# Performance work log

Hardware: AMD Instinct MI355X
Metric: run time of the kernel (lower is better)

Reference implementation:

```python
import jax, jax.numpy as jnp
import numpy as np

U, I, N, E, F, H, TOPK = 2048, 16384, 18432, 1_000_000, 64, 32, 3
NEG = -1e30  # stands in for 'structural zero' entries excluded from top-k


def setup_inputs() -> dict:
    key = jax.random.key(0)
    ks = jax.random.split(key, 6)
    x = jax.random.normal(ks[0], (N, F), dtype=jnp.float32)
    w1 = jax.random.normal(ks[1], (H, 2 * F + 2), dtype=jnp.float32) * 0.1
    b1 = jnp.zeros((H,), dtype=jnp.float32)
    w2 = jax.random.normal(ks[2], (1, H), dtype=jnp.float32) * 0.1
    b2 = jnp.zeros((1,), dtype=jnp.float32)
    edge_src = jax.random.randint(ks[3], (E,), 0, U)        # user-local == global (user_idx = arange)
    edge_dst_item = jax.random.randint(ks[4], (E,), 0, I)   # item-local; global item id = U + item
    user_idx = jnp.arange(U, dtype=jnp.int64) if jax.config.jax_enable_x64 else jnp.arange(U, dtype=jnp.int32)
    return {"x": x, "w1": w1, "b1": b1, "w2": w2, "b2": b2,
            "edge_src": edge_src, "edge_dst_item": edge_dst_item,
            "user_idx": user_idx, "num_nodes": N}


def reference(x, w1, b1, w2, b2, edge_src, edge_dst_item, user_idx, num_nodes):
    num_users = user_idx.shape[0]
    num_items = num_nodes - num_users
    u_local = edge_src           # user_idx = arange(U) so user_map is identity
    i_local = edge_dst_item      # item nodes occupy indices [U, N)

    ones = jnp.ones(u_local.shape[0], dtype=jnp.float32)
    d_u = jnp.log1p(jax.ops.segment_sum(ones, u_local, num_segments=num_users))  # [U]
    d_i = jnp.log1p(jax.ops.segment_sum(ones, i_local, num_segments=num_items))  # [I]

    # per-edge features: [u_x, log1p(deg_u), i_x, log1p(deg_i)] -> [E, 2F+2]
    x_u = x[user_idx[u_local]]
    x_it = x[num_users + i_local]
    x_e = jnp.concatenate([x_u, d_u[u_local][:, None], x_it, d_i[i_local][:, None]], axis=1)
    h = jax.nn.relu(x_e @ w1.T + b1)
    w = jax.nn.sigmoid(h @ w2.T + b2)[:, 0]  # [E], edge weights in (0,1)

    # A' [U, I] (duplicate edges coalesce-summed), C = A' A'^T with degree scaling
    A = jnp.zeros((num_users, num_items), dtype=jnp.float32).at[u_local, i_local].add(w)
    C = A @ A.T
    Dh = jnp.sqrt(d_u)
    C = C * Dh[:, None] * Dh[None, :]

    # per-row top-k restricted to structural nonzeros (all weights > 0)
    Cm = jnp.where(C > 0, C, NEG)
    vals, idx = jax.lax.top_k(Cm, TOPK)          # [U, K]
    valid = vals > 0
    vhalf = jnp.where(valid, vals, 0.0) * 0.5
    rows = jnp.broadcast_to(jnp.arange(num_users)[:, None], (num_users, TOPK))
    T = jnp.zeros((num_users, num_users), dtype=jnp.float32).at[rows, idx].add(vhalf)
    S = T + T.T  # symmetrized, deduped-by-sum adjacency; S[r,c] = val of edge (r,c)
    return S, d_u
```

## Files before the change

kernel.cpp:

```cpp
#include <hip/hip_runtime.h>
#include <hip/hip_bf16.h>
#include <math.h>

#define U_N 2048
#define I_N 16384
#define F_N 64
#define H_N 32
#define KDIM 16384
#define NEGV (-1e30f)
#define NB_DEG 256

typedef __attribute__((ext_vector_type(4))) float f32x4;

__device__ __forceinline__ void gload16(const void* g, void* l) {
    __builtin_amdgcn_global_load_lds(
        (const __attribute__((address_space(1))) unsigned int*)g,
        (__attribute__((address_space(3))) unsigned int*)l, 16, 0, 0);
}

__global__ __launch_bounds__(256) void k_deg_part(const int* __restrict__ src,
                                                  const int* __restrict__ dst, int E,
                                                  unsigned int* __restrict__ pu,
                                                  unsigned int* __restrict__ pi2,
                                                  float* __restrict__ C,
                                                  float* __restrict__ out) {
    __shared__ unsigned int hu[U_N];
    __shared__ unsigned int hi2[I_N / 2];
    int tid = threadIdx.x;
    for (int t = tid; t < U_N; t += 256) hu[t] = 0u;
    for (int t = tid; t < I_N / 2; t += 256) hi2[t] = 0u;
    __syncthreads();
    const int4* s4 = (const int4*)src;
    const int4* d4 = (const int4*)dst;
    int nv = E >> 2;
    for (int v = blockIdx.x * 256 + tid; v < nv; v += NB_DEG * 256) {
        int4 u = s4[v], i = d4[v];
        atomicAdd(&hu[u.x], 1u); atomicAdd(&hi2[i.x >> 1], 1u << ((i.x & 1) * 16));
        atomicAdd(&hu[u.y], 1u); atomicAdd(&hi2[i.y >> 1], 1u << ((i.y & 1) * 16));
        atomicAdd(&hu[u.z], 1u); atomicAdd(&hi2[i.z >> 1], 1u << ((i.z & 1) * 16));
        atomicAdd(&hu[u.w], 1u); atomicAdd(&hi2[i.w >> 1], 1u << ((i.w & 1) * 16));
    }
    if (blockIdx.x == 0) {
        int e = nv * 4 + tid;
        if (e < E) {
            atomicAdd(&hu[src[e]], 1u);
            int i = dst[e];
            atomicAdd(&hi2[i >> 1], 1u << ((i & 1) * 16));
        }
    }
    __syncthreads();
    unsigned int* pub = pu + (size_t)blockIdx.x * U_N;
    unsigned int* pib = pi2 + (size_t)blockIdx.x * (I_N / 2);
    for (int t = tid; t < U_N; t += 256) pub[t] = hu[t];
    for (int t = tid; t < I_N / 2; t += 256) pib[t] = hi2[t];
    const float4 z4 = {0.f, 0.f, 0.f, 0.f};
    float4* C4 = (float4*)C;
    for (int t = blockIdx.x * 256 + tid; t < U_N * U_N / 4; t += NB_DEG * 256)
        C4[t] = z4;
    float4* o4 = (float4*)out;
    for (int t = blockIdx.x * 256 + tid; t < (U_N * U_N + U_N) / 4; t += NB_DEG * 256)
        o4[t] = z4;
}

__global__ __launch_bounds__(256) void k_node2(const unsigned int* __restrict__ pu,
                                               const unsigned int* __restrict__ pi2,
                                               float* __restrict__ du,
                                               float* __restrict__ di,
                                               float* __restrict__ Dh,
                                               float* __restrict__ out_du,
                                               unsigned int* __restrict__ degu) {
    __shared__ unsigned int red[8][32];
    int j = threadIdx.x >> 5, l = threadIdx.x & 31;
    int e = blockIdx.x * 32 + l;
    unsigned int s = 0;
    if (e < U_N) {
        const unsigned int* p = pu + e;
#pragma unroll
        for (int k = 0; k < 32; ++k) s += p[(size_t)(j * 32 + k) * U_N];
    } else {
        const unsigned int* p = pi2 + (e - U_N);
#pragma unroll
        for (int k = 0; k < 32; ++k) s += p[(size_t)(j * 32 + k) * (I_N / 2)];
    }
    red[j][l] = s;
    __syncthreads();
    if (threadIdx.x < 32) {
        unsigned int t = 0;
#pragma unroll
        for (int jj = 0; jj < 8; ++jj) t += red[jj][l];
        if (e < U_N) {
            degu[e] = t;
            float v = log1pf((float)t);
            du[e] = v;
            Dh[e] = sqrtf(v);
            out_du[e] = v;
        } else {
            int ii = e - U_N;
            di[2 * ii]     = log1pf((float)(t & 0xffffu));
            di[2 * ii + 1] = log1pf((float)(t >> 16));
        }
    }
}

__global__ __launch_bounds__(256) void k_pof(const unsigned int* __restrict__ pu,
                                             const unsigned int* __restrict__ degu,
                                             unsigned int* __restrict__ base,
                                             unsigned int* __restrict__ pof) {
    __shared__ unsigned int dg[U_N];
    __shared__ unsigned int wt[4];
    __shared__ unsigned int ps[8][32];
    int tid = threadIdx.x;
    int wave = tid >> 6, lane = tid & 63;
    for (int t = tid; t < U_N; t += 256) dg[t] = degu[t];
    __syncthreads();
    unsigned int loc[8];
    unsigned int s = 0;
#pragma unroll
    for (int j = 0; j < 8; ++j) { loc[j] = dg[tid * 8 + j]; s += loc[j]; }
    unsigned int inc = s;
#pragma unroll
    for (int off = 1; off < 64; off <<= 1) {
        unsigned int o = __shfl_up(inc, off);
        if (lane >= off) inc += o;
    }
    if (lane == 63) wt[wave] = inc;
    __syncthreads();
    unsigned int woff = 0;
#pragma unroll
    for (int w = 0; w < 4; ++w) woff += (w < wave) ? wt[w] : 0u;
    unsigned int ex = woff + inc - s;
    __syncthreads();
    {
        unsigned int run = ex;
#pragma unroll
        for (int j = 0; j < 8; ++j) { unsigned int v = loc[j]; dg[tid * 8 + j] = run; run += v; }
    }
    __syncthreads();
    int c = tid >> 5, l = tid & 31;
    int u = blockIdx.x * 32 + l;
    if (c == 0) base[u] = dg[u];
    unsigned int v32[32];
    unsigned int sum = 0;
#pragma unroll
    for (int k = 0; k < 32; ++k) {
        v32[k] = pu[(size_t)(c * 32 + k) * U_N + u];
        sum += v32[k];
    }
    ps[c][l] = sum;
    __syncthreads();
    unsigned int run = dg[u];
#pragma unroll
    for (int c2 = 0; c2 < 8; ++c2) run += (c2 < c) ? ps[c2][l] : 0u;
#pragma unroll
    for (int k = 0; k < 32; ++k) {
        pof[(size_t)(c * 32 + k) * U_N + u] = run;
        run += v32[k];
    }
}

#define NPROJ (((U_N + I_N) * H_N) / 256)
__global__ __launch_bounds__(256) void k_pe(const int* __restrict__ src,
                                            const int* __restrict__ dst, int E,
                                            const unsigned int* __restrict__ pof,
                                            unsigned short* __restrict__ sorted,
                                            const float* __restrict__ x,
                                            const float* __restrict__ w1,
                                            const float* __restrict__ b1,
                                            const float* __restrict__ du,
                                            const float* __restrict__ di,
                                            float* __restrict__ Pu,
                                            float* __restrict__ Pi) {
    __shared__ unsigned int cur[U_N];
    int tid = threadIdx.x;
    int bid = blockIdx.x;
    if (bid < NB_DEG) {
        const unsigned int* p = pof + (size_t)bid * U_N;
        for (int t = tid; t < U_N; t += 256) cur[t] = p[t];
        __syncthreads();
        const int4* s4 = (const int4*)src;
        const int4* d4 = (const int4*)dst;
        int nv = E >> 2;
        for (int v = bid * 256 + tid; v < nv; v += NB_DEG * 256) {
            int4 u = s4[v], i = d4[v];
            sorted[atomicAdd(&cur[u.x], 1u)] = (unsigned short)i.x;
            sorted[atomicAdd(&cur[u.y], 1u)] = (unsigned short)i.y;
            sorted[atomicAdd(&cur[u.z], 1u)] = (unsigned short)i.z;
            sorted[atomicAdd(&cur[u.w], 1u)] = (unsigned short)i.w;
        }
        if (bid == 0) {
            int e = nv * 4 + tid;
            if (e < E)
                sorted[atomicAdd(&cur[src[e]], 1u)] = (unsigned short)dst[e];
        }
    } else {
        int t = (bid - NB_DEG) * 256 + tid;
        if (t < U_N * H_N) {
            int u = t >> 5, j = t & 31;
            const float* xr = x + (size_t)u * F_N;
            const float* wr = w1 + (size_t)j * (2 * F_N + 2);
            float acc = b1[j] + du[u] * wr[64];
#pragma unroll
            for (int f = 0; f < F_N; ++f) acc = fmaf(xr[f], wr[f], acc);
            Pu[t] = acc;
        } else {
            int t2 = t - U_N * H_N;
            int i = t2 >> 5, j = t2 & 31;
            const float* xr = x + (size_t)(U_N + i) * F_N;
            const float* wr = w1 + (size_t)j * (2 * F_N + 2) + 65;
            float acc = di[i] * wr[64];
#pragma unroll
            for (int f = 0; f < F_N; ++f) acc = fmaf(xr[f], wr[f], acc);
            Pi[t2] = acc;
        }
    }
}

__global__ __launch_bounds__(256) void k_edge2(const unsigned short* __restrict__ sorted,
                                               const unsigned int* __restrict__ base,
                                               const unsigned int* __restrict__ degu,
                                               const float* __restrict__ Pu,
                                               const float* __restrict__ Pi,
                                               const float* __restrict__ w2,
                                               const float* __restrict__ b2,
                                               unsigned int* __restrict__ A8w,
                                               float* __restrict__ diag) {
    __shared__ float hrow[I_N];
    __shared__ float red[256];
    int u = blockIdx.x, tid = threadIdx.x;
    float4* h4 = (float4*)hrow;
    float4 z4 = {0.f, 0.f, 0.f, 0.f};
#pragma unroll
    for (int j = 0; j < 16; ++j) h4[tid + j * 256] = z4;

    float pur[H_N], w2r[H_N];
#pragma unroll
    for (int j = 0; j < H_N; ++j) pur[j] = Pu[(size_t)u * H_N + j];
#pragma unroll
    for (int j = 0; j < H_N; ++j) w2r[j] = w2[j];
    float bb = b2[0];
    __syncthreads();

    int nb = (int)base[u], d = (int)degu[u];
    for (int k = tid; k < d; k += 256) {
        int i = (int)sorted[nb + k];
        const float4* pi4 = (const float4*)(Pi + (size_t)i * H_N);
        float acc = bb;
#pragma unroll
        for (int q = 0; q < H_N / 4; ++q) {
            float4 b = pi4[q];
            acc = fmaf(fmaxf(pur[4 * q + 0] + b.x, 0.f), w2r[4 * q + 0], acc);
            acc = fmaf(fmaxf(pur[4 * q + 1] + b.y, 0.f), w2r[4 * q + 1], acc);
            acc = fmaf(fmaxf(pur[4 * q + 2] + b.z, 0.f), w2r[4 * q + 2], acc);
            acc = fmaf(fmaxf(pur[4 * q + 3] + b.w, 0.f), w2r[4 * q + 3], acc);
        }
        float wgt = 1.0f / (1.0f + expf(-acc));
        atomicAdd(&hrow[i], wgt);
    }
    __syncthreads();

    unsigned int* row = A8w + (size_t)u * (I_N / 4);
    float ss = 0.f;
#pragma unroll
    for (int j = 0; j < 16; ++j) {
        int w = tid + j * 256;
        float4 a = h4[w];
        int v = __builtin_amdgcn_cvt_pk_fp8_f32(a.x, a.y, 0, false);
        v = __builtin_amdgcn_cvt_pk_fp8_f32(a.z, a.w, v, true);
        row[w] = (unsigned int)v;
        ss = fmaf(a.x, a.x, ss); ss = fmaf(a.y, a.y, ss);
        ss = fmaf(a.z, a.z, ss); ss = fmaf(a.w, a.w, ss);
    }
    red[tid] = ss;
    __syncthreads();
#pragma unroll
    for (int s = 128; s > 0; s >>= 1) {
        if (tid < s) red[tid] += red[tid + s];
        __syncthreads();
    }
    if (tid == 0) diag[u] = red[0];
}

#define BM 128
#define BKB 128
#define NBLK (U_N / BM)
#define NPAIR (NBLK * (NBLK + 1) / 2)
#define KSPLIT 4
#define KCH (KDIM / KSPLIT)

__global__ __launch_bounds__(256) void k_syrk(const unsigned char* __restrict__ A8,
                                              float* __restrict__ C) {
    __shared__ unsigned char As[BM * BKB];
    __shared__ unsigned char Bs[BM * BKB];

    int k0 = blockIdx.x * KCH;
    int p = blockIdx.y;
    int bi = 0, rem = p;
    while (rem >= NBLK - bi) { rem -= NBLK - bi; ++bi; }
    int bj = bi + rem;
    int diagp = (bi == bj);

    int tid = threadIdx.x;
    int wave = tid >> 6, lane = tid & 63;

    int srow = wave * 32 + (lane >> 3);
    int scol = ((lane & 7) ^ (lane >> 3)) * 16;
    const unsigned char* Ag = A8 + (size_t)(bi * BM + srow) * KDIM + k0 + scol;
    const unsigned char* Bg = A8 + (size_t)(bj * BM + srow) * KDIM + k0 + scol;
    unsigned char* lA = As + (wave * 32) * BKB;
    unsigned char* lB = Bs + (wave * 32) * BKB;

    int wm = wave >> 1, wn = wave & 1;
    int lm = lane & 15, lq = lane >> 4;
    int lm7 = lm & 7;
    const unsigned char* bTile = diagp ? As : Bs;

    f32x4 acc[4][4];
#pragma unroll
    for (int m = 0; m < 4; ++m)
#pragma unroll
        for (int n = 0; n < 4; ++n) acc[m][n] = (f32x4){0.f, 0.f, 0.f, 0.f};

    for (int kt = 0; kt < KCH; kt += BKB) {
        __syncthreads();
#pragma unroll
        for (int j = 0; j < 4; ++j)
            gload16(Ag + kt + (size_t)(j * 8) * KDIM, lA + j * 8 * BKB);
        if (!diagp) {
#pragma unroll
            for (int j = 0; j < 4; ++j)
                gload16(Bg + kt + (size_t)(j * 8) * KDIM, lB + j * 8 * BKB);
        }
        __syncthreads();

#pragma unroll
        for (int s = 0; s < 4; ++s) {
            int off = ((s * 2 + (lq >> 1)) ^ lm7) * 16 + (lq & 1) * 8;
            long av[4], bv[4];
#pragma unroll
            for (int m = 0; m < 4; ++m)
                av[m] = *(const long*)(As + (wm * 64 + m * 16 + lm) * BKB + off);
#pragma unroll
            for (int n = 0; n < 4; ++n)
                bv[n] = *(const long*)(bTile + (wn * 64 + n * 16 + lm) * BKB + off);
#pragma unroll
            for (int m = 0; m < 4; ++m)
#pragma unroll
                for (int n = 0; n < 4; ++n)
                    acc[m][n] = __builtin_amdgcn_mfma_f32_16x16x32_fp8_fp8(
                        av[m], bv[n], acc[m][n], 0, 0, 0);
        }
    }

#pragma unroll
    for (int m = 0; m < 4; ++m) {
        int rb = bi * BM + wm * 64 + m * 16 + lq * 4;
#pragma unroll
        for (int n = 0; n < 4; ++n) {
            int c = bj * BM + wn * 64 + n * 16 + lm;
            f32x4 v = acc[m][n];
#pragma unroll
            for (int g = 0; g < 4; ++g)
                atomicAdd(&C[(size_t)(rb + g) * U_N + c], v[g]);
        }
    }
}

__global__ __launch_bounds__(256) void k_mirror(float* __restrict__ C) {
    __shared__ float T[64][65];
    int tr = blockIdx.x, tc = blockIdx.y;
    if ((tr >> 1) <= (tc >> 1)) return;
    int lane = threadIdx.x & 63;
    int w = threadIdx.x >> 6;
#pragma unroll
    for (int s = 0; s < 16; ++s) {
        int r = s * 4 + w;
        T[r][lane] = C[(size_t)(tc * 64 + r) * U_N + tr * 64 + lane];
    }
    __syncthreads();
#pragma unroll
    for (int s = 0; s < 16; ++s) {
        int r = s * 4 + w;
        C[(size_t)(tr * 64 + r) * U_N + tc * 64 + lane] = T[lane][r];
    }
}

__device__ __forceinline__ bool better(float va, int ia, float vb, int ib) {
    return (va > vb) || (va == vb && ia < ib);
}
__device__ __forceinline__ void ins3(float v, int i, float& v0, int& i0,
                                     float& v1, int& i1, float& v2, int& i2) {
    if (better(v, i, v0, i0)) { v2 = v1; i2 = i1; v1 = v0; i1 = i0; v0 = v; i0 = i; }
    else if (better(v, i, v1, i1)) { v2 = v1; i2 = i1; v1 = v; i1 = i; }
    else if (better(v, i, v2, i2)) { v2 = v; i2 = i; }
}

__global__ __launch_bounds__(256) void k_topk(const float* __restrict__ C,
                                              const float* __restrict__ Dh,
                                              const float* __restrict__ diag,
                                              float* __restrict__ out) {
    int wave = threadIdx.x >> 6, lane = threadIdx.x & 63;
    int r = blockIdx.x * 4 + wave;
    float dr = Dh[r];
    float dex = diag[r] * dr * dr;
    float dval = (dex > 0.f) ? dex : NEGV;
    const float4* row = (const float4*)(C + (size_t)r * U_N);
    const float4* dh4 = (const float4*)Dh;
    float v0 = NEGV, v1 = NEGV, v2 = NEGV;
    int i0 = 0x7fffffff, i1 = 0x7fffffff, i2 = 0x7fffffff;
    int qr = r >> 2;
    for (int q = lane; q < U_N / 4; q += 64) {
        float4 cv = row[q];
        float4 dv = dh4[q];
        int c = q * 4;
        float x0 = (cv.x > 0.f) ? cv.x * dr * dv.x : NEGV;
        float x1 = (cv.y > 0.f) ? cv.y * dr * dv.y : NEGV;
        float x2 = (cv.z > 0.f) ? cv.z * dr * dv.z : NEGV;
        float x3 = (cv.w > 0.f) ? cv.w * dr * dv.w : NEGV;
        if (q == qr) {
            int j = r & 3;
            if (j == 0) x0 = dval; else if (j == 1) x1 = dval;
            else if (j == 2) x2 = dval; else x3 = dval;
        }
        if (better(x0, c + 0, v2, i2)) ins3(x0, c + 0, v0, i0, v1, i1, v2, i2);
        if (better(x1, c + 1, v2, i2)) ins3(x1, c + 1, v0, i0, v1, i1, v2, i2);
        if (better(x2, c + 2, v2, i2)) ins3(x2, c + 2, v0, i0, v1, i1, v2, i2);
        if (better(x3, c + 3, v2, i2)) ins3(x3, c + 3, v0, i0, v1, i1, v2, i2);
    }
#pragma unroll
    for (int off = 1; off < 64; off <<= 1) {
        float ov0 = __shfl_xor(v0, off), ov1 = __shfl_xor(v1, off), ov2 = __shfl_xor(v2, off);
        int oi0 = __shfl_xor(i0, off), oi1 = __shfl_xor(i1, off), oi2 = __shfl_xor(i2, off);
        ins3(ov0, oi0, v0, i0, v1, i1, v2, i2);
        ins3(ov1, oi1, v0, i0, v1, i1, v2, i2);
        ins3(ov2, oi2, v0, i0, v1, i1, v2, i2);
    }
    if (lane == 0) {
        float vs[3] = {v0, v1, v2};
        int is[3] = {i0, i1, i2};
#pragma unroll
        for (int k = 0; k < 3; ++k) {
            if (vs[k] > 0.f) {
                atomicAdd(&out[(size_t)r * U_N + is[k]], 0.5f * vs[k]);
                atomicAdd(&out[(size_t)is[k] * U_N + r], 0.5f * vs[k]);
            }
        }
    }
}

extern "C" void kernel_launch(void* const* d_in, const int* in_sizes, int n_in,
                              void* d_out, int out_size, void* d_ws, size_t ws_size,
                              hipStream_t stream) {
    const float* x  = (const float*)d_in[0];
    const float* w1 = (const float*)d_in[1];
    const float* b1 = (const float*)d_in[2];
    const float* w2 = (const float*)d_in[3];
    const float* b2 = (const float*)d_in[4];
    const int* esrc = (const int*)d_in[5];
    const int* edst = (const int*)d_in[6];
    int E = in_sizes[5];
    float* out = (float*)d_out;

    unsigned char* A8 = (unsigned char*)d_ws;
    float* C    = (float*)(A8 + (size_t)U_N * I_N);
    float* Pu   = C + (size_t)U_N * U_N;
    float* Pi   = Pu + (size_t)U_N * H_N;
    unsigned int* pu  = (unsigned int*)(Pi + (size_t)I_N * H_N);
    unsigned int* pi2 = pu + (size_t)NB_DEG * U_N;
    unsigned int* pof = pi2 + (size_t)NB_DEG * (I_N / 2);
    unsigned int* degu = pof + (size_t)NB_DEG * U_N;
    unsigned int* base = degu + U_N;
    float* du   = (float*)(base + U_N);
    float* di   = du + U_N;
    float* Dh   = di + I_N;
    float* diag = Dh + U_N;
    unsigned short* sorted = (unsigned short*)(diag + U_N);

    k_deg_part<<<NB_DEG, 256, 0, stream>>>(esrc, edst, E, pu, pi2, C, out);
    k_node2<<<(U_N + I_N / 2) / 32, 256, 0, stream>>>(pu, pi2, du, di, Dh,
                                                      out + (size_t)U_N * U_N, degu);
    k_pof<<<U_N / 32, 256, 0, stream>>>(pu, degu, base, pof);
    k_pe<<<NB_DEG + NPROJ, 256, 0, stream>>>(esrc, edst, E, pof, sorted,
                                             x, w1, b1, du, di, Pu, Pi);
    k_edge2<<<U_N, 256, 0, stream>>>(sorted, base, degu, Pu, Pi, w2, b2,
                                     (unsigned int*)A8, diag);
    k_syrk<<<dim3(KSPLIT, NPAIR), 256, 0, stream>>>(A8, C);
    k_mirror<<<dim3(U_N / 64, U_N / 64), 256, 0, stream>>>(C);
    k_topk<<<U_N / 4, 256, 0, stream>>>(C, Dh, diag, out);
}
```

Measured before the change: 284.1 us.

## Load SYRK MFMA operands directly from global memory, drop LDS staging

```diff
diff --git a/kernel.cpp b/kernel.cpp
--- a/kernel.cpp
+++ b/kernel.cpp
@@ -11,12 +11,6 @@
 #define NB_DEG 256
 
 typedef __attribute__((ext_vector_type(4))) float f32x4;
-
-__device__ __forceinline__ void gload16(const void* g, void* l) {
-    __builtin_amdgcn_global_load_lds(
-        (const __attribute__((address_space(1))) unsigned int*)g,
-        (__attribute__((address_space(3))) unsigned int*)l, 16, 0, 0);
-}
 
 __global__ __launch_bounds__(256) void k_deg_part(const int* __restrict__ src,
                                                   const int* __restrict__ dst, int E,
@@ -281,7 +275,6 @@
 }
 
 #define BM 128
-#define BKB 128
 #define NBLK (U_N / BM)
 #define NPAIR (NBLK * (NBLK + 1) / 2)
 #define KSPLIT 4
@@ -289,30 +282,25 @@
 
 __global__ __launch_bounds__(256) void k_syrk(const unsigned char* __restrict__ A8,
                                               float* __restrict__ C) {
-    __shared__ unsigned char As[BM * BKB];
-    __shared__ unsigned char Bs[BM * BKB];
-
     int k0 = blockIdx.x * KCH;
     int p = blockIdx.y;
     int bi = 0, rem = p;
     while (rem >= NBLK - bi) { rem -= NBLK - bi; ++bi; }
     int bj = bi + rem;
-    int diagp = (bi == bj);
 
     int tid = threadIdx.x;
     int wave = tid >> 6, lane = tid & 63;
-
-    int srow = wave * 32 + (lane >> 3);
-    int scol = ((lane & 7) ^ (lane >> 3)) * 16;
-    const unsigned char* Ag = A8 + (size_t)(bi * BM + srow) * KDIM + k0 + scol;
-    const unsigned char* Bg = A8 + (size_t)(bj * BM + srow) * KDIM + k0 + scol;
-    unsigned char* lA = As + (wave * 32) * BKB;
-    unsigned char* lB = Bs + (wave * 32) * BKB;
-
     int wm = wave >> 1, wn = wave & 1;
     int lm = lane & 15, lq = lane >> 4;
-    int lm7 = lm & 7;
-    const unsigned char* bTile = diagp ? As : Bs;
+
+    const unsigned char* aB[4];
+    const unsigned char* bB[4];
+#pragma unroll
+    for (int m = 0; m < 4; ++m)
+        aB[m] = A8 + (size_t)(bi * BM + wm * 64 + m * 16 + lm) * KDIM + k0 + lq * 8;
+#pragma unroll
+    for (int n = 0; n < 4; ++n)
+        bB[n] = A8 + (size_t)(bj * BM + wn * 64 + n * 16 + lm) * KDIM + k0 + lq * 8;
 
     f32x4 acc[4][4];
 #pragma unroll
@@ -320,35 +308,19 @@
 #pragma unroll
         for (int n = 0; n < 4; ++n) acc[m][n] = (f32x4){0.f, 0.f, 0.f, 0.f};
 
-    for (int kt = 0; kt < KCH; kt += BKB) {
-        __syncthreads();
-#pragma unroll
-        for (int j = 0; j < 4; ++j)
-            gload16(Ag + kt + (size_t)(j * 8) * KDIM, lA + j * 8 * BKB);
-        if (!diagp) {
-#pragma unroll
-            for (int j = 0; j < 4; ++j)
-                gload16(Bg + kt + (size_t)(j * 8) * KDIM, lB + j * 8 * BKB);
-        }
-        __syncthreads();
-
-#pragma unroll
-        for (int s = 0; s < 4; ++s) {
-            int off = ((s * 2 + (lq >> 1)) ^ lm7) * 16 + (lq & 1) * 8;
-            long av[4], bv[4];
-#pragma unroll
-            for (int m = 0; m < 4; ++m)
-                av[m] = *(const long*)(As + (wm * 64 + m * 16 + lm) * BKB + off);
+#pragma unroll 4
+    for (int kt = 0; kt < KCH; kt += 32) {
+        long av[4], bv[4];
+#pragma unroll
+        for (int m = 0; m < 4; ++m) av[m] = *(const long*)(aB[m] + kt);
+#pragma unroll
+        for (int n = 0; n < 4; ++n) bv[n] = *(const long*)(bB[n] + kt);
+#pragma unroll
+        for (int m = 0; m < 4; ++m)
 #pragma unroll
             for (int n = 0; n < 4; ++n)
-                bv[n] = *(const long*)(bTile + (wn * 64 + n * 16 + lm) * BKB + off);
-#pragma unroll
-            for (int m = 0; m < 4; ++m)
-#pragma unroll
-                for (int n = 0; n < 4; ++n)
-                    acc[m][n] = __builtin_amdgcn_mfma_f32_16x16x32_fp8_fp8(
-                        av[m], bv[n], acc[m][n], 0, 0, 0);
-        }
+                acc[m][n] = __builtin_amdgcn_mfma_f32_16x16x32_fp8_fp8(
+                    av[m], bv[n], acc[m][n], 0, 0, 0);
     }
 
 #pragma unroll
```

Result: slower. 542.8 us (+91.1%).
